# Kernel tuning notes

Hardware: AMD Instinct MI355X
Metric: run time of the kernel (lower is better)

Reference implementation:

```python
import jax, jax.numpy as jnp
import numpy as np

N_WIRES = 8
DIM = 2 ** N_WIRES  # 256 amplitudes
# PauliZ sign table: Z_SIGNS[w, i] = +1 if bit w of basis index i is 0 else -1
_bits = (np.arange(DIM)[None, :] >> (N_WIRES - 1 - np.arange(N_WIRES))[:, None]) & 1
Z_SIGNS = jnp.asarray(1.0 - 2.0 * _bits, dtype=jnp.float32)  # [8, 256]


def quantum_project(t, theta):
    """Batched 8-wire circuit: RX(x_w) encoder + trainable RX(theta_w) (RX gates on the
    same wire compose additively), then CNOT ring, then <Z_w> for each wire.
    t: [B, S, E] -> returns [B, S, H, 8]."""
    B, S, E = t.shape
    H = E // N_WIRES
    ang = (t.reshape(B, S, H, N_WIRES) + theta) * 0.5  # RX(a)RX(b)=RX(a+b)
    q0 = jnp.cos(ang).astype(jnp.complex64)
    q1 = (-1j * jnp.sin(ang)).astype(jnp.complex64)
    # Build product state |psi> = \otimes_w [cos(a_w/2), -i sin(a_w/2)] -> [B,S,H,256]
    state = jnp.ones((B, S, H, 1), jnp.complex64)
    for w in range(N_WIRES):
        qb = jnp.stack([q0[..., w], q1[..., w]], axis=-1)  # [B,S,H,2]
        state = (state[..., :, None] * qb[..., None, :]).reshape(B, S, H, -1)
    state = state.reshape((B, S, H) + (2,) * N_WIRES)  # wire w on axis 3+w
    # CNOT chain 0->1,...,6->7 then ring-closing 7->0
    for cw, tw in [(w, w + 1) for w in range(N_WIRES - 1)] + [(N_WIRES - 1, 0)]:
        s0 = jax.lax.index_in_dim(state, 0, axis=3 + cw, keepdims=True)
        s1 = jnp.flip(jax.lax.index_in_dim(state, 1, axis=3 + cw, keepdims=True), axis=3 + tw)
        state = jnp.concatenate([s0, s1], axis=3 + cw)
    amps = state.reshape(B, S, H, DIM)
    probs = amps.real * amps.real + amps.imag * amps.imag  # [B,S,H,256] float32
    return jnp.einsum('bshd,wd->bshw', probs, Z_SIGNS)  # <Z_w> per wire


def setup_inputs() -> dict:
    key = jax.random.key(0)
    kx, kq, kk, kv, ko, kt = jax.random.split(key, 6)
    B, S, E = 16, 512, 64
    scale = 1.0 / np.sqrt(E)
    return {
        'x': jax.random.normal(kx, (B, S, E), dtype=jnp.float32),
        'Wq': jax.random.normal(kq, (E, E), dtype=jnp.float32) * scale,
        'Wk': jax.random.normal(kk, (E, E), dtype=jnp.float32) * scale,
        'Wv': jax.random.normal(kv, (E, E), dtype=jnp.float32) * scale,
        'Wo': jax.random.normal(ko, (E, E), dtype=jnp.float32) * scale,
        'theta': jax.random.uniform(kt, (N_WIRES,), dtype=jnp.float32, minval=0.0, maxval=2.0 * np.pi),
    }


def reference(x, Wq, Wk, Wv, Wo, theta):
    B, S, E = x.shape
    q = quantum_project(x @ Wq.T, theta)  # [B,S,H,8]
    k = quantum_project(x @ Wk.T, theta)
    v = quantum_project(x @ Wv.T, theta)
    # NOTE: original code never transposes heads to dim 1, so attention mixes HEADS
    # per token: scores [B,S,H,H]. Faithfully reproduced. d_k = 8.
    scores = jnp.einsum('bsiw,bsjw->bsij', q, k) / jnp.float32(np.sqrt(N_WIRES))
    attn = jax.nn.softmax(scores, axis=-1)  # dropout is identity in eval
    out = jnp.einsum('bsij,bsjw->bsiw', attn, v)  # [B,S,H,8]
    # original: out.transpose(1,2).contiguous().view(B,-1,E) -> scrambled layout
    out = out.transpose(0, 2, 1, 3).reshape(B, -1, E)
    return out @ Wo.T
```

## Files before the change

kernel.cpp:

```cpp
#include <hip/hip_runtime.h>


typedef float  f32x4  __attribute__((ext_vector_type(4)));
typedef short  bf16x8 __attribute__((ext_vector_type(8)));
typedef unsigned short u16;
typedef unsigned int   u32;

#define WRS 72
#define SPS 68

#define DPP_SHR_STEP(d, j, sh)                                                 \
    {                                                                          \
        float _t = __int_as_float(__builtin_amdgcn_update_dpp(                 \
            0x3f800000, __float_as_int(d), 0x110 + sh, 0xf, 0xf, false));      \
        d *= ((j) >= (sh)) ? _t : 1.0f;                                        \
    }

__device__ __forceinline__ u32 bfh(float f) {
    const u32 u = __float_as_uint(f);
    return (u + 0x7FFFu + ((u >> 16) & 1u)) >> 16;
}
__device__ __forceinline__ void bfsplit(float f, u32& h, u32& l) {
    h = bfh(f);
    l = bfh(f - __uint_as_float(h << 16));
}

#define MFMA3(acc, ah, al, bh, bl)                                             \
    acc = __builtin_amdgcn_mfma_f32_16x16x32_bf16(al, bh, acc, 0, 0, 0);       \
    acc = __builtin_amdgcn_mfma_f32_16x16x32_bf16(ah, bl, acc, 0, 0, 0);       \
    acc = __builtin_amdgcn_mfma_f32_16x16x32_bf16(ah, bh, acc, 0, 0, 0);

__global__ __launch_bounds__(512, 1)
void qattn_fused(const float* __restrict__ xg,
                 const float* __restrict__ wqg, const float* __restrict__ wkg,
                 const float* __restrict__ wvg, const float* __restrict__ wog,
                 const float* __restrict__ thg,
                 float* __restrict__ outg)
{
    __shared__ u16 sWh[4 * 64 * WRS];
    __shared__ u16 sWl[4 * 64 * WRS];
    __shared__ u16 sXh[32 * WRS];
    __shared__ u16 sXl[32 * WRS];
    __shared__ __align__(16) float sP[96 * SPS];
    __shared__ u16 sSh[32 * WRS];
    __shared__ u16 sSl[32 * WRS];

    const int tid  = threadIdx.x;
    const int lane = tid & 63;
    const int wg   = tid >> 6;
    const int l15  = lane & 15;
    const int quad = lane >> 4;
    const int j    = lane & 7;
    const int b    = blockIdx.x >> 4;
    const int grp  = blockIdx.x & 15;

    {
        const float* gm[4] = {wqg, wkg, wvg, wog};
        #pragma unroll
        for (int r = 0; r < 8; ++r) {
            const int m   = r >> 1;
            const int idx = (r & 1) * 512 + tid;
            const float4 v = ((const float4*)gm[m])[idx];
            const int e = idx >> 4, c = idx & 15;
            u32 h0, l0, h1, l1, h2, l2, h3, l3;
            bfsplit(v.x, h0, l0); bfsplit(v.y, h1, l1);
            bfsplit(v.z, h2, l2); bfsplit(v.w, h3, l3);
            const int o = (m * 64 + e) * WRS + 4 * c;
            *(uint2*)&sWh[o] = make_uint2(h0 | (h1 << 16), h2 | (h3 << 16));
            *(uint2*)&sWl[o] = make_uint2(l0 | (l1 << 16), l2 | (l3 << 16));
        }
    }
    {
        const float4 v = ((const float4*)(xg + (size_t)(b * 512 + grp * 32) * 64))[tid];
        const int t = tid >> 4, c = tid & 15;
        u32 h0, l0, h1, l1, h2, l2, h3, l3;
        bfsplit(v.x, h0, l0); bfsplit(v.y, h1, l1);
        bfsplit(v.z, h2, l2); bfsplit(v.w, h3, l3);
        const int o = t * WRS + 4 * c;
        *(uint2*)&sXh[o] = make_uint2(h0 | (h1 << 16), h2 | (h3 << 16));
        *(uint2*)&sXl[o] = make_uint2(l0 | (l1 << 16), l2 | (l3 << 16));
    }
    const float thf = thg[j];
    __syncthreads();

    #pragma unroll
    for (int ia = 0; ia < 3; ++ia) {
        const int aid = wg * 3 + ia;
        const int mt = aid & 1, nt = (aid >> 1) & 3, m = aid >> 3;
        const int arow = (mt * 16 + l15) * WRS + quad * 8;
        const int brow = (m * 64 + nt * 16 + l15) * WRS + quad * 8;
        const bf16x8 ah0 = *(const bf16x8*)&sXh[arow];
        const bf16x8 ah1 = *(const bf16x8*)&sXh[arow + 32];
        const bf16x8 al0 = *(const bf16x8*)&sXl[arow];
        const bf16x8 al1 = *(const bf16x8*)&sXl[arow + 32];
        const bf16x8 bh0 = *(const bf16x8*)&sWh[brow];
        const bf16x8 bh1 = *(const bf16x8*)&sWh[brow + 32];
        const bf16x8 bl0 = *(const bf16x8*)&sWl[brow];
        const bf16x8 bl1 = *(const bf16x8*)&sWl[brow + 32];
        f32x4 acc = {0.f, 0.f, 0.f, 0.f};
        MFMA3(acc, ah0, al0, bh0, bl0)
        MFMA3(acc, ah1, al1, bh1, bl1)
        #pragma unroll
        for (int r = 0; r < 4; ++r) {
            const float c = __cosf(acc[r] + thf);
            float d = c;
            DPP_SHR_STEP(d, j, 1)
            DPP_SHR_STEP(d, j, 2)
            DPP_SHR_STEP(d, j, 4)
            float ex = (j == 0) ? 1.0f : c;
            DPP_SHR_STEP(ex, j, 1)
            DPP_SHR_STEP(ex, j, 2)
            DPP_SHR_STEP(ex, j, 4)
            const int row  = m * 32 + mt * 16 + quad * 4 + r;
            const int base = row * SPS + nt * 16 + l15;
            if (j > 0)  sP[base]     = d;
            if (j == 7) sP[base - 7] = ex;
        }
    }
    __syncthreads();

    if (wg < 4) {
        const int tg = wg * 8 + (lane >> 3);
        const int i  = j;
        const int qb = tg * SPS;
        const int kb = (32 + tg) * SPS;
        const int vb = (64 + tg) * SPS;
        float q[8];
        *(float4*)&q[0] = *(const float4*)&sP[qb + 8 * i];
        *(float4*)&q[4] = *(const float4*)&sP[qb + 8 * i + 4];
        float pr[8];
        float sum = 0.f;
        #pragma unroll
        for (int jj = 0; jj < 8; ++jj) {
            const float4 k0 = *(const float4*)&sP[kb + 8 * jj];
            const float4 k1 = *(const float4*)&sP[kb + 8 * jj + 4];
            float s = q[0] * k0.x;
            s = fmaf(q[1], k0.y, s); s = fmaf(q[2], k0.z, s);
            s = fmaf(q[3], k0.w, s); s = fmaf(q[4], k1.x, s);
            s = fmaf(q[5], k1.y, s); s = fmaf(q[6], k1.z, s);
            s = fmaf(q[7], k1.w, s);
            pr[jj] = __expf(s * 0.35355339059327373f);
            sum += pr[jj];
        }
        const float rinv = 1.0f / sum;
        float o[8];
        #pragma unroll
        for (int w = 0; w < 8; ++w) o[w] = 0.f;
        #pragma unroll
        for (int jj = 0; jj < 8; ++jj) {
            const float4 v0 = *(const float4*)&sP[vb + 8 * jj];
            const float4 v1 = *(const float4*)&sP[vb + 8 * jj + 4];
            const float a = pr[jj] * rinv;
            o[0] = fmaf(a, v0.x, o[0]); o[1] = fmaf(a, v0.y, o[1]);
            o[2] = fmaf(a, v0.z, o[2]); o[3] = fmaf(a, v0.w, o[3]);
            o[4] = fmaf(a, v1.x, o[4]); o[5] = fmaf(a, v1.y, o[5]);
            o[6] = fmaf(a, v1.z, o[6]); o[7] = fmaf(a, v1.w, o[7]);
        }
        u32 hh[4], ll[4];
        #pragma unroll
        for (int c = 0; c < 4; ++c) {
            u32 ha, la, hb, lb;
            bfsplit(o[2 * c], ha, la);
            bfsplit(o[2 * c + 1], hb, lb);
            hh[c] = ha | (hb << 16);
            ll[c] = la | (lb << 16);
        }
        const int so = (i * 4 + (tg >> 3)) * WRS + 8 * (tg & 7);
        *(uint4*)&sSh[so] = make_uint4(hh[0], hh[1], hh[2], hh[3]);
        *(uint4*)&sSl[so] = make_uint4(ll[0], ll[1], ll[2], ll[3]);
    }
    __syncthreads();

    {
        const int mt2 = wg >> 2, nt2 = wg & 3;
        const int arow = (mt2 * 16 + l15) * WRS + quad * 8;
        const int brow = (3 * 64 + nt2 * 16 + l15) * WRS + quad * 8;
        const bf16x8 ah0 = *(const bf16x8*)&sSh[arow];
        const bf16x8 ah1 = *(const bf16x8*)&sSh[arow + 32];
        const bf16x8 al0 = *(const bf16x8*)&sSl[arow];
        const bf16x8 al1 = *(const bf16x8*)&sSl[arow + 32];
        const bf16x8 bh0 = *(const bf16x8*)&sWh[brow];
        const bf16x8 bh1 = *(const bf16x8*)&sWh[brow + 32];
        const bf16x8 bl0 = *(const bf16x8*)&sWl[brow];
        const bf16x8 bl1 = *(const bf16x8*)&sWl[brow + 32];
        f32x4 acc = {0.f, 0.f, 0.f, 0.f};
        MFMA3(acc, ah0, al0, bh0, bl0)
        MFMA3(acc, ah1, al1, bh1, bl1)
        const int e = nt2 * 16 + l15;
        #pragma unroll
        for (int r = 0; r < 4; ++r) {
            const int rho = mt2 * 16 + quad * 4 + r;
            const int R   = (rho >> 2) * 64 + grp * 4 + (rho & 3);
            outg[((size_t)(b * 512 + R)) * 64 + e] = acc[r];
        }
    }
}

extern "C" void kernel_launch(void* const* d_in, const int* in_sizes, int n_in,
                              void* d_out, int out_size, void* d_ws, size_t ws_size,
                              hipStream_t stream) {
    const float* x  = (const float*)d_in[0];
    const float* wq = (const float*)d_in[1];
    const float* wk = (const float*)d_in[2];
    const float* wv = (const float*)d_in[3];
    const float* wo = (const float*)d_in[4];
    const float* th = (const float*)d_in[5];
    float* out = (float*)d_out;
    qattn_fused<<<dim3(256), dim3(512), 0, stream>>>(x, wq, wk, wv, wo, th, out);
}
```

Measured before the change: 67.11 us.

## Load weights directly into MFMA registers and halve tokens per block

Drops the shared-memory staging of all four weight matrices and the input tile. Each lane now loads and splits its own fragments straight from global memory into bf16 hi/lo registers. The block shrinks to 256 threads handling 16 tokens, so there are 512 blocks and two can share a CU, and the hi/lo bf16 split uses a cheaper truncate-and-perm routine. This removes the upfront weight staging and a barrier per block, at the cost of redundant global weight reads across waves and blocks (served from cache) and a slightly different rounding of the split.

```diff
diff --git a/kernel.cpp b/kernel.cpp
--- a/kernel.cpp
+++ b/kernel.cpp
@@ -16,13 +16,25 @@
         d *= ((j) >= (sh)) ? _t : 1.0f;                                        \
     }
 
-__device__ __forceinline__ u32 bfh(float f) {
-    const u32 u = __float_as_uint(f);
-    return (u + 0x7FFFu + ((u >> 16) & 1u)) >> 16;
+__device__ __forceinline__ void bfsplit2(float f0, float f1, u32& hh, u32& ll) {
+    const u32 u0 = __float_as_uint(f0), u1 = __float_as_uint(f1);
+    const u32 h0 = (u0 + 0x8000u) & 0xffff0000u;
+    const u32 h1 = (u1 + 0x8000u) & 0xffff0000u;
+    const float r0 = f0 - __uint_as_float(h0);
+    const float r1 = f1 - __uint_as_float(h1);
+    hh = __builtin_amdgcn_perm(h1, h0, 0x07060302u);
+    ll = __builtin_amdgcn_perm(__float_as_uint(r1), __float_as_uint(r0),
+                               0x07060302u);
 }
-__device__ __forceinline__ void bfsplit(float f, u32& h, u32& l) {
-    h = bfh(f);
-    l = bfh(f - __uint_as_float(h << 16));
+
+__device__ __forceinline__ void cvt8(const float4 v0, const float4 v1,
+                                     bf16x8& hi, bf16x8& lo) {
+    union { bf16x8 v; u32 u[4]; } H, L;
+    bfsplit2(v0.x, v0.y, H.u[0], L.u[0]);
+    bfsplit2(v0.z, v0.w, H.u[1], L.u[1]);
+    bfsplit2(v1.x, v1.y, H.u[2], L.u[2]);
+    bfsplit2(v1.z, v1.w, H.u[3], L.u[3]);
+    hi = H.v; lo = L.v;
 }
 
 #define MFMA3(acc, ah, al, bh, bl)                                             \
@@ -30,20 +42,16 @@
     acc = __builtin_amdgcn_mfma_f32_16x16x32_bf16(ah, bl, acc, 0, 0, 0);       \
     acc = __builtin_amdgcn_mfma_f32_16x16x32_bf16(ah, bh, acc, 0, 0, 0);
 
-__global__ __launch_bounds__(512, 1)
+__global__ __launch_bounds__(256, 2)
 void qattn_fused(const float* __restrict__ xg,
                  const float* __restrict__ wqg, const float* __restrict__ wkg,
                  const float* __restrict__ wvg, const float* __restrict__ wog,
                  const float* __restrict__ thg,
                  float* __restrict__ outg)
 {
-    __shared__ u16 sWh[4 * 64 * WRS];
-    __shared__ u16 sWl[4 * 64 * WRS];
-    __shared__ u16 sXh[32 * WRS];
-    __shared__ u16 sXl[32 * WRS];
-    __shared__ __align__(16) float sP[96 * SPS];
-    __shared__ u16 sSh[32 * WRS];
-    __shared__ u16 sSl[32 * WRS];
+    __shared__ __align__(16) float sP[48 * SPS];
+    __shared__ __align__(16) u16 sSh[16 * WRS];
+    __shared__ __align__(16) u16 sSl[16 * WRS];
 
     const int tid  = threadIdx.x;
     const int lane = tid & 63;
@@ -51,52 +59,24 @@
     const int l15  = lane & 15;
     const int quad = lane >> 4;
     const int j    = lane & 7;
-    const int b    = blockIdx.x >> 4;
-    const int grp  = blockIdx.x & 15;
+    const int b    = blockIdx.x >> 5;
+    const int g16  = blockIdx.x & 31;
 
-    {
-        const float* gm[4] = {wqg, wkg, wvg, wog};
-        #pragma unroll
-        for (int r = 0; r < 8; ++r) {
-            const int m   = r >> 1;
-            const int idx = (r & 1) * 512 + tid;
-            const float4 v = ((const float4*)gm[m])[idx];
-            const int e = idx >> 4, c = idx & 15;
-            u32 h0, l0, h1, l1, h2, l2, h3, l3;
-            bfsplit(v.x, h0, l0); bfsplit(v.y, h1, l1);
-            bfsplit(v.z, h2, l2); bfsplit(v.w, h3, l3);
-            const int o = (m * 64 + e) * WRS + 4 * c;
-            *(uint2*)&sWh[o] = make_uint2(h0 | (h1 << 16), h2 | (h3 << 16));
-            *(uint2*)&sWl[o] = make_uint2(l0 | (l1 << 16), l2 | (l3 << 16));
-        }
-    }
-    {
-        const float4 v = ((const float4*)(xg + (size_t)(b * 512 + grp * 32) * 64))[tid];
-        const int t = tid >> 4, c = tid & 15;
-        u32 h0, l0, h1, l1, h2, l2, h3, l3;
-        bfsplit(v.x, h0, l0); bfsplit(v.y, h1, l1);
-        bfsplit(v.z, h2, l2); bfsplit(v.w, h3, l3);
-        const int o = t * WRS + 4 * c;
-        *(uint2*)&sXh[o] = make_uint2(h0 | (h1 << 16), h2 | (h3 << 16));
-        *(uint2*)&sXl[o] = make_uint2(l0 | (l1 << 16), l2 | (l3 << 16));
-    }
+    const float* xr = xg + ((size_t)(b * 512 + g16 * 16 + l15) * 64) + quad * 8;
+    bf16x8 ah0, al0, ah1, al1;
+    cvt8(*(const float4*)xr, *(const float4*)(xr + 4), ah0, al0);
+    cvt8(*(const float4*)(xr + 32), *(const float4*)(xr + 36), ah1, al1);
     const float thf = thg[j];
-    __syncthreads();
 
     #pragma unroll
     for (int ia = 0; ia < 3; ++ia) {
         const int aid = wg * 3 + ia;
-        const int mt = aid & 1, nt = (aid >> 1) & 3, m = aid >> 3;
-        const int arow = (mt * 16 + l15) * WRS + quad * 8;
-        const int brow = (m * 64 + nt * 16 + l15) * WRS + quad * 8;
-        const bf16x8 ah0 = *(const bf16x8*)&sXh[arow];
-        const bf16x8 ah1 = *(const bf16x8*)&sXh[arow + 32];
-        const bf16x8 al0 = *(const bf16x8*)&sXl[arow];
-        const bf16x8 al1 = *(const bf16x8*)&sXl[arow + 32];
-        const bf16x8 bh0 = *(const bf16x8*)&sWh[brow];
-        const bf16x8 bh1 = *(const bf16x8*)&sWh[brow + 32];
-        const bf16x8 bl0 = *(const bf16x8*)&sWl[brow];
-        const bf16x8 bl1 = *(const bf16x8*)&sWl[brow + 32];
+        const int m = aid >> 2, nt = aid & 3;
+        const float* wm = (m == 0) ? wqg : ((m == 1) ? wkg : wvg);
+        const float* wr = wm + (nt * 16 + l15) * 64 + quad * 8;
+        bf16x8 bh0, bl0, bh1, bl1;
+        cvt8(*(const float4*)wr, *(const float4*)(wr + 4), bh0, bl0);
+        cvt8(*(const float4*)(wr + 32), *(const float4*)(wr + 36), bh1, bl1);
         f32x4 acc = {0.f, 0.f, 0.f, 0.f};
         MFMA3(acc, ah0, al0, bh0, bl0)
         MFMA3(acc, ah1, al1, bh1, bl1)
@@ -111,20 +91,25 @@
             DPP_SHR_STEP(ex, j, 1)
             DPP_SHR_STEP(ex, j, 2)
             DPP_SHR_STEP(ex, j, 4)
-            const int row  = m * 32 + mt * 16 + quad * 4 + r;
-            const int base = row * SPS + nt * 16 + l15;
+            const int base = (m * 16 + quad * 4 + r) * SPS + nt * 16 + l15;
             if (j > 0)  sP[base]     = d;
             if (j == 7) sP[base - 7] = ex;
         }
     }
+
+    const float* wor = wog + (wg * 16 + l15) * 64 + quad * 8;
+    bf16x8 obh0, obl0, obh1, obl1;
+    cvt8(*(const float4*)wor, *(const float4*)(wor + 4), obh0, obl0);
+    cvt8(*(const float4*)(wor + 32), *(const float4*)(wor + 36), obh1, obl1);
+
     __syncthreads();
 
-    if (wg < 4) {
+    if (wg < 2) {
         const int tg = wg * 8 + (lane >> 3);
         const int i  = j;
         const int qb = tg * SPS;
-        const int kb = (32 + tg) * SPS;
-        const int vb = (64 + tg) * SPS;
+        const int kb = (16 + tg) * SPS;
+        const int vb = (32 + tg) * SPS;
         float q[8];
         *(float4*)&q[0] = *(const float4*)&sP[qb + 8 * i];
         *(float4*)&q[4] = *(const float4*)&sP[qb + 8 * i + 4];
@@ -158,39 +143,28 @@
         }
         u32 hh[4], ll[4];
         #pragma unroll
-        for (int c = 0; c < 4; ++c) {
-            u32 ha, la, hb, lb;
-            bfsplit(o[2 * c], ha, la);
-            bfsplit(o[2 * c + 1], hb, lb);
-            hh[c] = ha | (hb << 16);
-            ll[c] = la | (lb << 16);
-        }
-        const int so = (i * 4 + (tg >> 3)) * WRS + 8 * (tg & 7);
+        for (int c = 0; c < 4; ++c)
+            bfsplit2(o[2 * c], o[2 * c + 1], hh[c], ll[c]);
+        const int so = (i * 2 + (tg >> 3)) * WRS + 8 * (tg & 7);
         *(uint4*)&sSh[so] = make_uint4(hh[0], hh[1], hh[2], hh[3]);
         *(uint4*)&sSl[so] = make_uint4(ll[0], ll[1], ll[2], ll[3]);
     }
     __syncthreads();
 
     {
-        const int mt2 = wg >> 2, nt2 = wg & 3;
-        const int arow = (mt2 * 16 + l15) * WRS + quad * 8;
-        const int brow = (3 * 64 + nt2 * 16 + l15) * WRS + quad * 8;
-        const bf16x8 ah0 = *(const bf16x8*)&sSh[arow];
-        const bf16x8 ah1 = *(const bf16x8*)&sSh[arow + 32];
-        const bf16x8 al0 = *(const bf16x8*)&sSl[arow];
-        const bf16x8 al1 = *(const bf16x8*)&sSl[arow + 32];
-        const bf16x8 bh0 = *(const bf16x8*)&sWh[brow];
-        const bf16x8 bh1 = *(const bf16x8*)&sWh[brow + 32];
-        const bf16x8 bl0 = *(const bf16x8*)&sWl[brow];
-        const bf16x8 bl1 = *(const bf16x8*)&sWl[brow + 32];
+        const int arow = l15 * WRS + quad * 8;
+        const bf16x8 sh0 = *(const bf16x8*)&sSh[arow];
+        const bf16x8 sh1 = *(const bf16x8*)&sSh[arow + 32];
+        const bf16x8 sl0 = *(const bf16x8*)&sSl[arow];
+        const bf16x8 sl1 = *(const bf16x8*)&sSl[arow + 32];
         f32x4 acc = {0.f, 0.f, 0.f, 0.f};
-        MFMA3(acc, ah0, al0, bh0, bl0)
-        MFMA3(acc, ah1, al1, bh1, bl1)
-        const int e = nt2 * 16 + l15;
+        MFMA3(acc, sh0, sl0, obh0, obl0)
+        MFMA3(acc, sh1, sl1, obh1, obl1)
+        const int e = wg * 16 + l15;
         #pragma unroll
         for (int r = 0; r < 4; ++r) {
-            const int rho = mt2 * 16 + quad * 4 + r;
-            const int R   = (rho >> 2) * 64 + grp * 4 + (rho & 3);
+            const int rho = quad * 4 + r;
+            const int R   = (rho >> 1) * 64 + g16 * 2 + (rho & 1);
             outg[((size_t)(b * 512 + R)) * 64 + e] = acc[r];
         }
     }
@@ -206,5 +180,5 @@
     const float* wo = (const float*)d_in[4];
     const float* th = (const float*)d_in[5];
     float* out = (float*)d_out;
-    qattn_fused<<<dim3(256), dim3(512), 0, stream>>>(x, wq, wk, wv, wo, th, out);
+    qattn_fused<<<dim3(512), dim3(256), 0, stream>>>(x, wq, wk, wv, wo, th, out);
 }
```

New measurement: 70.00 us. 4.3% more time.
